# Performance work log

Hardware: AMD Instinct MI355X
Metric: run time of the kernel (lower is better)

Reference implementation:

```python
import jax, jax.numpy as jnp
import numpy as np

EPS = 1e-5
NUM_GROUPS = 32


def group_norm(x, scale, bias):
    # x: [B, C, H, W], 32 groups, normalized over (C/G, H, W)
    B, C, H, W = x.shape
    G = NUM_GROUPS
    xg = x.reshape(B, G, C // G, H, W)
    mean = xg.mean(axis=(2, 3, 4), keepdims=True)
    var = xg.var(axis=(2, 3, 4), keepdims=True)
    xg = (xg - mean) * jax.lax.rsqrt(var + EPS)
    x = xg.reshape(B, C, H, W)
    return x * scale[None, :, None, None] + bias[None, :, None, None]


def setup_inputs() -> dict:
    key = jax.random.key(0)
    ks = jax.random.split(key, 6)
    B, C, H, W = 32, 512, 32, 32
    std = 1.0 / np.sqrt(C)
    return {
        "x": jax.random.normal(ks[0], (B, C, H, W), dtype=jnp.float32),
        "gn_scale": jnp.ones((C,), dtype=jnp.float32),
        "gn_bias": jnp.zeros((C,), dtype=jnp.float32),
        "wq": jax.random.normal(ks[1], (C, C), dtype=jnp.float32) * std,
        "bq": jnp.zeros((C,), dtype=jnp.float32),
        "wk": jax.random.normal(ks[2], (C, C), dtype=jnp.float32) * std,
        "bk": jnp.zeros((C,), dtype=jnp.float32),
        "wv": jax.random.normal(ks[3], (C, C), dtype=jnp.float32) * std,
        "bv": jnp.zeros((C,), dtype=jnp.float32),
        "wo": jax.random.normal(ks[4], (C, C), dtype=jnp.float32) * std,
        "bo": jnp.zeros((C,), dtype=jnp.float32),
    }


def reference(x, gn_scale, gn_bias, wq, bq, wk, bk, wv, bv, wo, bo):
    B, C, H, W = x.shape
    h = group_norm(x, gn_scale, gn_bias)
    # 1x1 convs == per-pixel matmuls; flatten spatial to tokens: [B, HW, C]
    ht = h.reshape(B, C, H * W).transpose(0, 2, 1)
    q = jnp.einsum('bnc,oc->bno', ht, wq) + bq  # [B, HW, C]
    k = jnp.einsum('bnc,oc->bno', ht, wk) + bk
    v = jnp.einsum('bnc,oc->bno', ht, wv) + bv
    scale = 1.0 / jnp.sqrt(jnp.asarray(C, x.dtype))
    w = jnp.einsum('bnc,bmc->bnm', q, k) * scale  # [B, HW, HW]
    w = jax.nn.softmax(w, axis=-1)
    a = jnp.einsum('bnm,bmc->bnc', w, v)  # [B, HW, C]
    out = jnp.einsum('bnc,oc->bno', a, wo) + bo
    out = out.transpose(0, 2, 1).reshape(B, C, H, W)
    return x + out
```

## Files before the change

### kernel.cpp

```cpp
#include <hip/hip_runtime.h>
#include <hip/hip_bf16.h>
#include <stdint.h>

typedef unsigned short u16;
typedef __attribute__((ext_vector_type(8))) short short8;
typedef __attribute__((ext_vector_type(4))) short s16x4;
typedef __attribute__((ext_vector_type(4))) float f32x4;

#define NTOK 1024
#define CDIM 512
#define NG 32

#define GLOAD_LDS16(gptr, lptr)                                                              \
  __builtin_amdgcn_global_load_lds((const __attribute__((address_space(1))) unsigned int*)(gptr), \
                                   (__attribute__((address_space(3))) unsigned int*)(lptr), 16, 0, 0)

__device__ __forceinline__ u16 f2bf(float f) {
  __hip_bfloat16 h = __float2bfloat16(f);
  union { __hip_bfloat16 h; u16 u; } v; v.h = h;
  return v.u;
}

__device__ __forceinline__ float bf2f(u16 b) {
  union { uint32_t u; float f; } v; v.u = ((uint32_t)b) << 16;
  return v.f;
}

__global__ __launch_bounds__(256) void prep_stats(const float* __restrict__ x,
                                                  const float* __restrict__ wq, const float* __restrict__ wk,
                                                  const float* __restrict__ wv, const float* __restrict__ wo,
                                                  const float* __restrict__ bq, const float* __restrict__ bk,
                                                  const float* __restrict__ bv,
                                                  u16* __restrict__ wout, float* __restrict__ bqkv,
                                                  float* __restrict__ rsum,
                                                  float* __restrict__ mean_o, float* __restrict__ rstd_o) {
  int bg = blockIdx.x;
  int i = bg * 256 + threadIdx.x;
  wout[i]          = f2bf(wq[i]);
  wout[262144 + i] = f2bf(wk[i]);
  wout[524288 + i] = f2bf(wv[i]);
  wout[786432 + i] = f2bf(wo[i]);
  if (i < 512) bqkv[i] = bq[i];
  else if (i < 1024) bqkv[i] = bk[i - 512];
  else if (i < 1536) bqkv[i] = bv[i - 1024];
  if (i < 32768) rsum[i] = 0.f;

  const float4* base = (const float4*)(x + (size_t)bg * 16384);
  float s = 0.f, ss = 0.f;
  for (int k = threadIdx.x; k < 4096; k += 256) {
    float4 v = base[k];
    s  += v.x + v.y + v.z + v.w;
    ss += v.x * v.x + v.y * v.y + v.z * v.z + v.w * v.w;
  }
#pragma unroll
  for (int d = 1; d < 64; d <<= 1) { s += __shfl_xor(s, d); ss += __shfl_xor(ss, d); }
  __shared__ float as[4], as2[4];
  int w = threadIdx.x >> 6;
  if ((threadIdx.x & 63) == 0) { as[w] = s; as2[w] = ss; }
  __syncthreads();
  if (threadIdx.x == 0) {
    float S = as[0] + as[1] + as[2] + as[3];
    float SS = as2[0] + as2[1] + as2[2] + as2[3];
    float m = S * (1.f / 16384.f);
    float var = SS * (1.f / 16384.f) - m * m;
    mean_o[bg] = m;
    rstd_o[bg] = rsqrtf(var + 1e-5f);
  }
}

__global__ __launch_bounds__(256) void gn_apply(const float* __restrict__ x,
                                                const float* __restrict__ mean_, const float* __restrict__ rstd_,
                                                const float* __restrict__ gsc, const float* __restrict__ gbi,
                                                u16* __restrict__ h) {
  int n0 = blockIdx.x * 64, c0 = blockIdx.y * 64, b = blockIdx.z;
  __shared__ u16 t[64][65];
  int tid = threadIdx.x;
  int nl4 = (tid & 15) * 4;
  int clb = tid >> 4;
#pragma unroll
  for (int p = 0; p < 4; ++p) {
    int cl = p * 16 + clb;
    int c = c0 + cl;
    int g = c >> 4;
    float m = mean_[b * NG + g], rs = rstd_[b * NG + g];
    float sc = gsc[c] * rs, bi = gbi[c] - m * sc;
    float4 v = *(const float4*)(x + ((size_t)b * CDIM + c) * NTOK + n0 + nl4);
    t[cl][nl4 + 0] = f2bf(v.x * sc + bi);
    t[cl][nl4 + 1] = f2bf(v.y * sc + bi);
    t[cl][nl4 + 2] = f2bf(v.z * sc + bi);
    t[cl][nl4 + 3] = f2bf(v.w * sc + bi);
  }
  __syncthreads();
  int nl = tid >> 3;
  int cc = (tid & 7) * 8;
#pragma unroll
  for (int p = 0; p < 2; ++p) {
    int n = nl + p * 32;
    short8 o;
#pragma unroll
    for (int i = 0; i < 8; ++i) o[i] = (short)t[cc + i][n];
    *(short8*)(h + (size_t)(b * NTOK + n0 + n) * CDIM + c0 + cc) = o;
  }
}

template <int MODE>
__device__ __forceinline__ void gemm_body(const u16* __restrict__ A, const u16* __restrict__ B,
                                          const float* __restrict__ bias, u16* __restrict__ outb,
                                          u16* __restrict__ outb2,
                                          float* __restrict__ outf, const float* __restrict__ resid,
                                          int Ka, int Kb, int nkt,
                                          size_t strideA, size_t strideB, int batch0) {
  int nx = gridDim.x, ny = gridDim.y;
  int nwg = nx * ny * gridDim.z;
  int id = blockIdx.x + nx * (blockIdx.y + ny * blockIdx.z);
  int cpx = nwg >> 3;
  int sw = (id & 7) * cpx + (id >> 3);
  int bx = sw % nx; int t_ = sw / nx;
  int by = t_ % ny; int z = t_ / ny;

  const u16* Amat = A + (size_t)z * strideA;
  const u16* Bmat = B + (size_t)z * strideB;
  int n0 = bx * 256, m0 = by * 256;
  __shared__ __align__(16) u16 SH[65536];
  int tid = threadIdx.x;
  int l = tid & 63, wid = tid >> 6;
  int lr = l & 15, lh = l >> 4;
  int wm = (wid >> 2) * 128;
  int wn = (wid & 3) * 64;

  f32x4 acc[8][4];
#pragma unroll
  for (int i = 0; i < 8; ++i)
#pragma unroll
    for (int j = 0; j < 4; ++j) acc[i][j] = (f32x4){0.f, 0.f, 0.f, 0.f};

  short8 af[4][2];
  short8 bf01[2][2];
  short8 bf23[2][2];

  int sr = tid >> 3, sc = tid & 7;
  int sg = (sc ^ (sr & 7)) << 3;
  const u16* Ag0 = Amat + (size_t)(m0 + sr) * Ka + sg;
  const u16* Ag1 = Ag0 + (size_t)64 * Ka;
  const u16* Bg0 = Bmat + (size_t)(n0 + sr) * Kb + sg;
  const u16* Bg1 = Bg0 + (size_t)64 * Kb;
  size_t hA = (size_t)128 * Ka, hB = (size_t)128 * Kb;
  u16* Al0 = SH + sr * 64 + sc * 8;
  u16* Bl0 = SH + 32768 + sr * 64 + sc * 8;

#define STAGE_A(bufsel, ktv, half)                                        \
  {                                                                       \
    size_t go_ = (size_t)(ktv) * 64 + ((half) ? hA : (size_t)0);          \
    u16* ld_ = Al0 + (bufsel) * 16384 + (half) * 8192;                    \
    GLOAD_LDS16(Ag0 + go_, ld_);                                          \
    GLOAD_LDS16(Ag1 + go_, ld_ + 4096);                                   \
  }
#define STAGE_B(bufsel, ktv, half)                                        \
  {                                                                       \
    size_t go_ = (size_t)(ktv) * 64 + ((half) ? hB : (size_t)0);          \
    u16* ld_ = Bl0 + (bufsel) * 16384 + (half) * 8192;                    \
    GLOAD_LDS16(Bg0 + go_, ld_);                                          \
    GLOAD_LDS16(Bg1 + go_, ld_ + 4096);                                   \
  }

#define READ_AF(ihalf, bufsel)                                                        \
  _Pragma("unroll") for (int i_ = 0; i_ < 4; ++i_) {                                  \
    int row_ = wm + (ihalf) * 64 + i_ * 16 + lr;                                      \
    const u16* p_ = SH + (bufsel) * 16384 + row_ * 64;                                \
    _Pragma("unroll") for (int ks_ = 0; ks_ < 2; ++ks_)                               \
      af[i_][ks_] = *(const short8*)(p_ + (((ks_ * 4 + lh) ^ (row_ & 7)) << 3));      \
  }

#define READ_BF(dst, jbase, bufsel)                                                   \
  _Pragma("unroll") for (int j_ = 0; j_ < 2; ++j_) {                                  \
    int row_ = wn + ((jbase) + j_) * 16 + lr;                                         \
    const u16* p_ = SH + 32768 + (bufsel) * 16384 + row_ * 64;                        \
    _Pragma("unroll") for (int ks_ = 0; ks_ < 2; ++ks_)                               \
      dst[j_][ks_] = *(const short8*)(p_ + (((ks_ * 4 + lh) ^ (row_ & 7)) << 3));     \
  }

#define MFMA_Q(ihalf, jbase, bsrc)                                                    \
  _Pragma("unroll") for (int ks_ = 0; ks_ < 2; ++ks_)                                 \
    _Pragma("unroll") for (int i_ = 0; i_ < 4; ++i_)                                  \
      _Pragma("unroll") for (int j_ = 0; j_ < 2; ++j_)                                \
        acc[(ihalf) * 4 + i_][(jbase) + j_] = __builtin_amdgcn_mfma_f32_16x16x32_bf16( \
            af[i_][ks_], bsrc[j_][ks_], acc[(ihalf) * 4 + i_][(jbase) + j_], 0, 0, 0);

#define PBAR() __builtin_amdgcn_s_barrier()

#define PHASES(BC, BN, GI, DOHI, DOLO)                                    \
  {                                                                       \
    int g1_ = (GI) + 1, g2_ = (GI) + 2;                                   \
                                           \
    READ_AF(0, BC);                                                       \
    READ_BF(bf01, 0, BC);                                                 \
    if (DOHI) { STAGE_A(BN, g1_, 1); }                                    \
    PBAR();                                                               \
    __builtin_amdgcn_s_setprio(1);                                        \
    MFMA_Q(0, 0, bf01);                                                   \
    __builtin_amdgcn_s_setprio(0);                                        \
    PBAR();                                                               \
                                           \
    READ_BF(bf23, 2, BC);                                                 \
    if (DOHI) { STAGE_B(BN, g1_, 1); }                                    \
    PBAR();                                                               \
    __builtin_amdgcn_s_setprio(1);                                        \
    MFMA_Q(0, 2, bf23);                                                   \
    __builtin_amdgcn_s_setprio(0);                                        \
    PBAR();                                                               \
     \
    READ_AF(1, BC);                                                       \
    if (DOLO) { STAGE_B(BC, g2_, 0); }                                    \
    PBAR();                                                               \
    __builtin_amdgcn_s_setprio(1);                                        \
    MFMA_Q(1, 2, bf23);                                                   \
    __builtin_amdgcn_s_setprio(0);                                        \
    PBAR();                                                               \
     \
    if (DOLO) { STAGE_A(BC, g2_, 0); }                                    \
    PBAR();                                                               \
    __builtin_amdgcn_s_setprio(1);                                        \
    MFMA_Q(1, 0, bf01);                                                   \
    __builtin_amdgcn_s_setprio(0);                                        \
    if (DOLO) { asm volatile("s_waitcnt vmcnt(4)"); }                     \
    else      { asm volatile("s_waitcnt vmcnt(0)"); }                     \
    __builtin_amdgcn_sched_barrier(0);                                    \
    PBAR();                                                               \
  }

  int k1 = (1 < nkt) ? 1 : 0;
  STAGE_B(0, 0, 0);
  STAGE_A(0, 0, 0);
  STAGE_A(0, 0, 1);
  STAGE_B(0, 0, 1);
  STAGE_B(1, k1, 0);
  STAGE_A(1, k1, 0);
  asm volatile("s_waitcnt vmcnt(4)");
  __builtin_amdgcn_sched_barrier(0);
  PBAR();

  for (int kt = 0; kt < nkt; kt += 2) {
    int more = (kt + 2 < nkt) ? 1 : 0;
    PHASES(0, 1, kt, 1, more);
    PHASES(1, 0, kt + 1, more, more);
  }

  __syncthreads();
  const int gr0 = m0 + wm, gc0 = n0 + wn;
  u16* eb = SH + wid * 4352;

  if constexpr (MODE == 5) {
    float bj[4];
#pragma unroll
    for (int j = 0; j < 4; ++j) bj[j] = bias[gc0 + j * 16 + lr];
    if (n0 < 1024) {
#pragma unroll
      for (int pass = 0; pass < 2; ++pass) {
#pragma unroll
        for (int i2 = 0; i2 < 4; ++i2)
#pragma unroll
          for (int j = 0; j < 4; ++j)
#pragma unroll
            for (int r = 0; r < 4; ++r)
              eb[(i2 * 16 + lh * 4 + r) * 68 + j * 16 + lr] =
                  f2bf(acc[pass * 4 + i2][j][r] + bj[j]);
        asm volatile("s_waitcnt lgkmcnt(0)");
        __builtin_amdgcn_sched_barrier(0);
#pragma unroll
        for (int t = 0; t < 8; ++t) {
          int row = t * 8 + (l >> 3), c8 = (l & 7) * 8;
          s16x4 lo = *(const s16x4*)(eb + row * 68 + c8);
          s16x4 hi = *(const s16x4*)(eb + row * 68 + c8 + 4);
          short8 o;
          o[0] = lo[0]; o[1] = lo[1]; o[2] = lo[2]; o[3] = lo[3];
          o[4] = hi[0]; o[5] = hi[1]; o[6] = hi[2]; o[7] = hi[3];
          *(short8*)(outb + (size_t)(gr0 + pass * 64 + row) * 1024 + gc0 + c8) = o;
        }
        asm volatile("s_waitcnt lgkmcnt(0)");
        __builtin_amdgcn_sched_barrier(0);
      }
    } else {
      int ch0 = gc0 - 1024;
      int bt = m0 >> 10, tok0 = (m0 & 1023) + wm;
#pragma unroll
      for (int pass = 0; pass < 2; ++pass) {
#pragma unroll
        for (int i2 = 0; i2 < 4; ++i2)
#pragma unroll
          for (int j = 0; j < 4; ++j) {
            s16x4 w;
#pragma unroll
            for (int r = 0; r < 4; ++r)
              w[r] = (short)f2bf(acc[pass * 4 + i2][j][r] + bj[j]);
            *(s16x4*)(eb + (j * 16 + lr) * 68 + i2 * 16 + lh * 4) = w;
          }
        asm volatile("s_waitcnt lgkmcnt(0)");
        __builtin_amdgcn_sched_barrier(0);
#pragma unroll
        for (int t = 0; t < 8; ++t) {
          int row = t * 8 + (l >> 3), c8 = (l & 7) * 8;
          s16x4 lo = *(const s16x4*)(eb + row * 68 + c8);
          s16x4 hi = *(const s16x4*)(eb + row * 68 + c8 + 4);
          short8 o;
          o[0] = lo[0]; o[1] = lo[1]; o[2] = lo[2]; o[3] = lo[3];
          o[4] = hi[0]; o[5] = hi[1]; o[6] = hi[2]; o[7] = hi[3];
          *(short8*)(outb2 + (size_t)(bt * 512 + ch0 + row) * 1024 + tok0 + pass * 64 + c8) = o;
        }
        asm volatile("s_waitcnt lgkmcnt(0)");
        __builtin_amdgcn_sched_barrier(0);
      }
    }
  } else if constexpr (MODE == 3) {
    const float k2 = 0.063758716f;
    u16* obase = outb + (size_t)z * 1048576;
    float* rsb = outf + (size_t)z * 1024;
#pragma unroll
    for (int pass = 0; pass < 2; ++pass) {
#pragma unroll
      for (int i2 = 0; i2 < 4; ++i2)
#pragma unroll
        for (int r = 0; r < 4; ++r) {
          float rp = 0.f;
#pragma unroll
          for (int j = 0; j < 4; ++j) {
            float e = exp2f(acc[pass * 4 + i2][j][r] * k2);
            rp += e;
            eb[(i2 * 16 + lh * 4 + r) * 68 + j * 16 + lr] = f2bf(e);
          }
          rp += __shfl_xor(rp, 1);
          rp += __shfl_xor(rp, 2);
          rp += __shfl_xor(rp, 4);
          rp += __shfl_xor(rp, 8);
          if (lr == 0) atomicAdd(rsb + gr0 + pass * 64 + i2 * 16 + lh * 4 + r, rp);
        }
      asm volatile("s_waitcnt lgkmcnt(0)");
      __builtin_amdgcn_sched_barrier(0);
#pragma unroll
      for (int t = 0; t < 8; ++t) {
        int row = t * 8 + (l >> 3), c8 = (l & 7) * 8;
        s16x4 lo = *(const s16x4*)(eb + row * 68 + c8);
        s16x4 hi = *(const s16x4*)(eb + row * 68 + c8 + 4);
        short8 o;
        o[0] = lo[0]; o[1] = lo[1]; o[2] = lo[2]; o[3] = lo[3];
        o[4] = hi[0]; o[5] = hi[1]; o[6] = hi[2]; o[7] = hi[3];
        *(short8*)(obase + (size_t)(gr0 + pass * 64 + row) * 1024 + gc0 + c8) = o;
      }
      asm volatile("s_waitcnt lgkmcnt(0)");
      __builtin_amdgcn_sched_barrier(0);
    }
  } else if constexpr (MODE == 4) {
    const float* rsg = outf + (size_t)z * 1024;
    u16* obase = outb + (size_t)(batch0 + z) * 524288;
#pragma unroll
    for (int pass = 0; pass < 2; ++pass) {
#pragma unroll
      for (int i2 = 0; i2 < 4; ++i2)
#pragma unroll
        for (int r = 0; r < 4; ++r) {
          float inv_ = 1.f / rsg[gr0 + pass * 64 + i2 * 16 + lh * 4 + r];
#pragma unroll
          for (int j = 0; j < 4; ++j)
            eb[(i2 * 16 + lh * 4 + r) * 68 + j * 16 + lr] =
                f2bf(acc[pass * 4 + i2][j][r] * inv_);
        }
      asm volatile("s_waitcnt lgkmcnt(0)");
      __builtin_amdgcn_sched_barrier(0);
#pragma unroll
      for (int t = 0; t < 8; ++t) {
        int row = t * 8 + (l >> 3), c8 = (l & 7) * 8;
        s16x4 lo = *(const s16x4*)(eb + row * 68 + c8);
        s16x4 hi = *(const s16x4*)(eb + row * 68 + c8 + 4);
        short8 o;
        o[0] = lo[0]; o[1] = lo[1]; o[2] = lo[2]; o[3] = lo[3];
        o[4] = hi[0]; o[5] = hi[1]; o[6] = hi[2]; o[7] = hi[3];
        *(short8*)(obase + (size_t)(gr0 + pass * 64 + row) * 512 + gc0 + c8) = o;
      }
      asm volatile("s_waitcnt lgkmcnt(0)");
      __builtin_amdgcn_sched_barrier(0);
    }
  }
#undef STAGE_A
#undef STAGE_B
#undef READ_AF
#undef READ_BF
#undef MFMA_Q
#undef PBAR
#undef PHASES
}

__device__ __forceinline__ void gemm_body_o(const u16* __restrict__ A, const u16* __restrict__ B,
                                            const float* __restrict__ bias,
                                            float* __restrict__ outf, const float* __restrict__ resid,
                                            int Ka, int Kb, int nkt) {
  int nx = gridDim.x, ny = gridDim.y;
  int nwg = nx * ny;
  int id = blockIdx.x + nx * blockIdx.y;
  int cpx = nwg >> 3;
  int sw = (id & 7) * cpx + (id >> 3);
  int bx = sw % nx; int by = sw / nx;

  int n0 = bx * 128, m0 = by * 256;
  __shared__ __align__(16) u16 SH[36864];
  int tid = threadIdx.x;
  int l = tid & 63, wid = tid >> 6;
  int lr = l & 15, lh = l >> 4;
  int wm = (wid >> 1) * 128;
  int wn = (wid & 1) * 64;

  f32x4 acc[8][4];
#pragma unroll
  for (int i = 0; i < 8; ++i)
#pragma unroll
    for (int j = 0; j < 4; ++j) acc[i][j] = (f32x4){0.f, 0.f, 0.f, 0.f};

  short8 af[8];
  short8 bfr[4];

  int sr = tid >> 2, sc4 = tid & 3;
  int sg = (sc4 ^ ((sr >> 1) & 3)) * 8;
  const u16* Ag0 = A + (size_t)(m0 + sr) * Ka + sg;
  const u16* Bg0 = B + (size_t)(n0 + sr) * Kb + sg;
  u16* Al0 = SH + sr * 32 + sc4 * 8;
  u16* Bl0 = SH + 24576 + sr * 32 + sc4 * 8;

  int rch = (lh ^ ((lr >> 1) & 3)) * 8;

#define STG(bufsel, ktv)                                                          \
  {                                                                               \
    GLOAD_LDS16(Ag0 + (ktv) * 32,                       Al0 + (bufsel) * 8192);   \
    GLOAD_LDS16(Ag0 + (ktv) * 32 + (size_t)64  * Ka,    Al0 + (bufsel) * 8192 + 2048); \
    GLOAD_LDS16(Ag0 + (ktv) * 32 + (size_t)128 * Ka,    Al0 + (bufsel) * 8192 + 4096); \
    GLOAD_LDS16(Ag0 + (ktv) * 32 + (size_t)192 * Ka,    Al0 + (bufsel) * 8192 + 6144); \
    GLOAD_LDS16(Bg0 + (ktv) * 32,                       Bl0 + (bufsel) * 4096);   \
    GLOAD_LDS16(Bg0 + (ktv) * 32 + (size_t)64  * Kb,    Bl0 + (bufsel) * 4096 + 2048); \
  }

#define RDF(bufsel)                                                                   \
  _Pragma("unroll") for (int i_ = 0; i_ < 8; ++i_)                                    \
    af[i_] = *(const short8*)(SH + (bufsel) * 8192 + (wm + i_ * 16 + lr) * 32 + rch); \
  _Pragma("unroll") for (int j_ = 0; j_ < 4; ++j_)                                    \
    bfr[j_] = *(const short8*)(SH + 24576 + (bufsel) * 4096 + (wn + j_ * 16 + lr) * 32 + rch);

#define MFM32()                                                                       \
  _Pragma("unroll") for (int i_ = 0; i_ < 8; ++i_)                                    \
    _Pragma("unroll") for (int j_ = 0; j_ < 4; ++j_)                                  \
      acc[i_][j_] = __builtin_amdgcn_mfma_f32_16x16x32_bf16(af[i_], bfr[j_], acc[i_][j_], 0, 0, 0);

  STG(0, 0);
  STG(1, 1);
  asm volatile("s_waitcnt vmcnt(6)");
  __builtin_amdgcn_sched_barrier(0);
  __builtin_amdgcn_s_barrier();

  int bc = 0, bs = 2;
  for (int t = 0; t < nkt; ++t) {
    const bool more = (t + 2 < nkt);
    if (more) STG(bs, t + 2);
    RDF(bc);
    __builtin_amdgcn_s_setprio(1);
    MFM32();
    __builtin_amdgcn_s_setprio(0);
    if (more) { asm volatile("s_waitcnt vmcnt(6)"); }
    else      { asm volatile("s_waitcnt vmcnt(0)"); }
    __builtin_amdgcn_sched_barrier(0);
    __builtin_amdgcn_s_barrier();
    bc = (bc == 2) ? 0 : bc + 1;
    bs = (bs == 2) ? 0 : bs + 1;
  }

  __syncthreads();
  const int gr0 = m0 + wm, gc0 = n0 + wn;
  float* ebf = (float*)SH + wid * 2176;
  int bt = n0 >> 10, nn0 = (n0 & 1023) + wn;
#pragma unroll
  for (int pass = 0; pass < 4; ++pass) {
#pragma unroll
    for (int i2 = 0; i2 < 2; ++i2)
#pragma unroll
      for (int r = 0; r < 4; ++r) {
        float bv = bias[gr0 + pass * 32 + i2 * 16 + lh * 4 + r];
#pragma unroll
        for (int j = 0; j < 4; ++j)
          ebf[(i2 * 16 + lh * 4 + r) * 68 + j * 16 + lr] = acc[pass * 2 + i2][j][r] + bv;
      }
    asm volatile("s_waitcnt lgkmcnt(0)");
    __builtin_amdgcn_sched_barrier(0);
#pragma unroll
    for (int t = 0; t < 8; ++t) {
      int row = t * 4 + (l >> 4), c4 = (l & 15) * 4;
      float4 vv = *(const float4*)(ebf + row * 68 + c4);
      size_t addr = ((size_t)bt * 512 + gr0 + pass * 32 + row) * 1024 + nn0 + c4;
      const float4 rr = *(const float4*)(resid + addr);
      vv.x += rr.x; vv.y += rr.y; vv.z += rr.z; vv.w += rr.w;
      *(float4*)(outf + addr) = vv;
    }
    asm volatile("s_waitcnt lgkmcnt(0)");
    __builtin_amdgcn_sched_barrier(0);
  }
#undef STG
#undef RDF
#undef MFM32
}

__global__ __launch_bounds__(512, 2) void gemm_qkv(const u16* A, const u16* B, const float* bias,
                                                   u16* outb, u16* outb2, float* outf, const float* resid,
                                                   int Ka, int Kb, int nkt, size_t sA, size_t sB, int b0) {
  gemm_body<5>(A, B, bias, outb, outb2, outf, resid, Ka, Kb, nkt, sA, sB, b0);
}
__global__ __launch_bounds__(256, 2) void gemm_o(const u16* A, const u16* B, const float* bias,
                                                 float* outf, const float* resid,
                                                 int Ka, int Kb, int nkt) {
  gemm_body_o(A, B, bias, outf, resid, Ka, Kb, nkt);
}
__global__ __launch_bounds__(512, 2) void gemm_s(const u16* A, const u16* B, const float* bias,
                                                 u16* outb, u16* outb2, float* outf, const float* resid,
                                                 int Ka, int Kb, int nkt, size_t sA, size_t sB, int b0) {
  gemm_body<3>(A, B, bias, outb, outb2, outf, resid, Ka, Kb, nkt, sA, sB, b0);
}
__global__ __launch_bounds__(512, 2) void gemm_pv(const u16* A, const u16* B, const float* bias,
                                                  u16* outb, u16* outb2, float* outf, const float* resid,
                                                  int Ka, int Kb, int nkt, size_t sA, size_t sB, int b0) {
  gemm_body<4>(A, B, bias, outb, outb2, outf, resid, Ka, Kb, nkt, sA, sB, b0);
}

extern "C" void kernel_launch(void* const* d_in, const int* in_sizes, int n_in,
                              void* d_out, int out_size, void* d_ws, size_t ws_size,
                              hipStream_t stream) {
  const float* x   = (const float*)d_in[0];
  const float* gsc = (const float*)d_in[1];
  const float* gbi = (const float*)d_in[2];
  const float* wq  = (const float*)d_in[3];
  const float* bq  = (const float*)d_in[4];
  const float* wk  = (const float*)d_in[5];
  const float* bk  = (const float*)d_in[6];
  const float* wv  = (const float*)d_in[7];
  const float* bv  = (const float*)d_in[8];
  const float* wo  = (const float*)d_in[9];
  const float* bo  = (const float*)d_in[10];

  char* ws = (char*)d_ws;
  u16* wbf = (u16*)ws;
  float* bqkv = (float*)(ws + (2ull << 20));
  float* mean_ = (float*)(ws + (2ull << 20) + 65536);
  float* rstd_ = mean_ + 1024;
  float* rsum = (float*)(ws + (3ull << 20));
  u16* h   = (u16*)(ws + (4ull << 20));
  u16* qk  = (u16*)(ws + (36ull << 20));
  u16* vm  = (u16*)(ws + (100ull << 20));
  u16* S   = (u16*)(ws + (132ull << 20));
  u16* am  = h;
  float* out = (float*)d_out;

  size_t sbytes = ws_size > (132ull << 20) ? ws_size - (132ull << 20) : 0;
  int CB = 1;
  while (CB < 32 && (size_t)(CB * 2) * (2ull << 20) <= sbytes) CB *= 2;

  prep_stats<<<1024, 256, 0, stream>>>(x, wq, wk, wv, wo, bq, bk, bv, wbf, bqkv, rsum, mean_, rstd_);
  gn_apply<<<dim3(16, 8, 32), 256, 0, stream>>>(x, mean_, rstd_, gsc, gbi, h);
  gemm_qkv<<<dim3(6, 128), 512, 0, stream>>>(h, wbf, bqkv, qk, vm, nullptr, nullptr,
                                             512, 512, 8, 0, 0, 0);
  for (int c0 = 0; c0 < 32; c0 += CB) {
    gemm_s<<<dim3(4, 4, CB), 512, 0, stream>>>(qk + (size_t)c0 * 1048576, qk + 512 + (size_t)c0 * 1048576,
                                               nullptr, S, nullptr, rsum + (size_t)c0 * 1024, nullptr,
                                               1024, 1024, 8, 1048576, 1048576, 0);
    gemm_pv<<<dim3(2, 4, CB), 512, 0, stream>>>(S, vm + (size_t)c0 * 524288,
                                                nullptr, am, nullptr, rsum + (size_t)c0 * 1024, nullptr,
                                                1024, 1024, 16, 1048576, 524288, c0);
  }
  gemm_o<<<dim3(256, 2), 256, 0, stream>>>(wbf + 786432, am, bo, out, x, 512, 512, 16);
}
```

Measured before the change: 225.1 us.

## Fuse QK^T, exp, row-sum and PV into one flash-style attention kernel

Replaces the separate score GEMM (writing bf16 exp scores to a workspace) and PV GEMM with a single fused kernel that keeps 64-query tiles of Q in LDS, streams K and V tiles, computes exp scores and row sums locally, and accumulates P·V in registers. This removes the global round-trip of the 32x1024x1024 score matrix and the per-chunk launch loop. It uses no running max, as before, and the small 16x32 score tiles per wave with many barriers may limit MFMA utilisation.

Measured after the change: 332.8 us. 1.48x slower.

```diff
diff --git a/kernel.cpp b/kernel.cpp
--- a/kernel.cpp
+++ b/kernel.cpp
@@ -32,7 +32,6 @@
                                                   const float* __restrict__ bq, const float* __restrict__ bk,
                                                   const float* __restrict__ bv,
                                                   u16* __restrict__ wout, float* __restrict__ bqkv,
-                                                  float* __restrict__ rsum,
                                                   float* __restrict__ mean_o, float* __restrict__ rstd_o) {
   int bg = blockIdx.x;
   int i = bg * 256 + threadIdx.x;
@@ -43,7 +42,6 @@
   if (i < 512) bqkv[i] = bq[i];
   else if (i < 1024) bqkv[i] = bk[i - 512];
   else if (i < 1536) bqkv[i] = bv[i - 1024];
-  if (i < 32768) rsum[i] = 0.f;
 
   const float4* base = (const float4*)(x + (size_t)bg * 16384);
   float s = 0.f, ss = 0.f;
@@ -107,19 +105,14 @@
 __device__ __forceinline__ void gemm_body(const u16* __restrict__ A, const u16* __restrict__ B,
                                           const float* __restrict__ bias, u16* __restrict__ outb,
                                           u16* __restrict__ outb2,
-                                          float* __restrict__ outf, const float* __restrict__ resid,
-                                          int Ka, int Kb, int nkt,
-                                          size_t strideA, size_t strideB, int batch0) {
+                                          int Ka, int Kb, int nkt) {
   int nx = gridDim.x, ny = gridDim.y;
-  int nwg = nx * ny * gridDim.z;
-  int id = blockIdx.x + nx * (blockIdx.y + ny * blockIdx.z);
+  int nwg = nx * ny;
+  int id = blockIdx.x + nx * blockIdx.y;
   int cpx = nwg >> 3;
   int sw = (id & 7) * cpx + (id >> 3);
-  int bx = sw % nx; int t_ = sw / nx;
-  int by = t_ % ny; int z = t_ / ny;
-
-  const u16* Amat = A + (size_t)z * strideA;
-  const u16* Bmat = B + (size_t)z * strideB;
+  int bx = sw % nx; int by = sw / nx;
+
   int n0 = bx * 256, m0 = by * 256;
   __shared__ __align__(16) u16 SH[65536];
   int tid = threadIdx.x;
@@ -140,9 +133,9 @@
 
   int sr = tid >> 3, sc = tid & 7;
   int sg = (sc ^ (sr & 7)) << 3;
-  const u16* Ag0 = Amat + (size_t)(m0 + sr) * Ka + sg;
+  const u16* Ag0 = A + (size_t)(m0 + sr) * Ka + sg;
   const u16* Ag1 = Ag0 + (size_t)64 * Ka;
-  const u16* Bg0 = Bmat + (size_t)(n0 + sr) * Kb + sg;
+  const u16* Bg0 = B + (size_t)(n0 + sr) * Kb + sg;
   const u16* Bg1 = Bg0 + (size_t)64 * Kb;
   size_t hA = (size_t)128 * Ka, hB = (size_t)128 * Kb;
   u16* Al0 = SH + sr * 64 + sc * 8;
@@ -191,7 +184,6 @@
 #define PHASES(BC, BN, GI, DOHI, DOLO)                                    \
   {                                                                       \
     int g1_ = (GI) + 1, g2_ = (GI) + 2;                                   \
-                                           \
     READ_AF(0, BC);                                                       \
     READ_BF(bf01, 0, BC);                                                 \
     if (DOHI) { STAGE_A(BN, g1_, 1); }                                    \
@@ -200,7 +192,6 @@
     MFMA_Q(0, 0, bf01);                                                   \
     __builtin_amdgcn_s_setprio(0);                                        \
     PBAR();                                                               \
-                                           \
     READ_BF(bf23, 2, BC);                                                 \
     if (DOHI) { STAGE_B(BN, g1_, 1); }                                    \
     PBAR();                                                               \
@@ -208,7 +199,6 @@
     MFMA_Q(0, 2, bf23);                                                   \
     __builtin_amdgcn_s_setprio(0);                                        \
     PBAR();                                                               \
-     \
     READ_AF(1, BC);                                                       \
     if (DOLO) { STAGE_B(BC, g2_, 0); }                                    \
     PBAR();                                                               \
@@ -216,7 +206,6 @@
     MFMA_Q(1, 2, bf23);                                                   \
     __builtin_amdgcn_s_setprio(0);                                        \
     PBAR();                                                               \
-     \
     if (DOLO) { STAGE_A(BC, g2_, 0); }                                    \
     PBAR();                                                               \
     __builtin_amdgcn_s_setprio(1);                                        \
@@ -249,90 +238,20 @@
   const int gr0 = m0 + wm, gc0 = n0 + wn;
   u16* eb = SH + wid * 4352;
 
-  if constexpr (MODE == 5) {
-    float bj[4];
-#pragma unroll
-    for (int j = 0; j < 4; ++j) bj[j] = bias[gc0 + j * 16 + lr];
-    if (n0 < 1024) {
-#pragma unroll
-      for (int pass = 0; pass < 2; ++pass) {
-#pragma unroll
-        for (int i2 = 0; i2 < 4; ++i2)
-#pragma unroll
-          for (int j = 0; j < 4; ++j)
-#pragma unroll
-            for (int r = 0; r < 4; ++r)
-              eb[(i2 * 16 + lh * 4 + r) * 68 + j * 16 + lr] =
-                  f2bf(acc[pass * 4 + i2][j][r] + bj[j]);
-        asm volatile("s_waitcnt lgkmcnt(0)");
-        __builtin_amdgcn_sched_barrier(0);
-#pragma unroll
-        for (int t = 0; t < 8; ++t) {
-          int row = t * 8 + (l >> 3), c8 = (l & 7) * 8;
-          s16x4 lo = *(const s16x4*)(eb + row * 68 + c8);
-          s16x4 hi = *(const s16x4*)(eb + row * 68 + c8 + 4);
-          short8 o;
-          o[0] = lo[0]; o[1] = lo[1]; o[2] = lo[2]; o[3] = lo[3];
-          o[4] = hi[0]; o[5] = hi[1]; o[6] = hi[2]; o[7] = hi[3];
-          *(short8*)(outb + (size_t)(gr0 + pass * 64 + row) * 1024 + gc0 + c8) = o;
-        }
-        asm volatile("s_waitcnt lgkmcnt(0)");
-        __builtin_amdgcn_sched_barrier(0);
-      }
-    } else {
-      int ch0 = gc0 - 1024;
-      int bt = m0 >> 10, tok0 = (m0 & 1023) + wm;
-#pragma unroll
-      for (int pass = 0; pass < 2; ++pass) {
-#pragma unroll
-        for (int i2 = 0; i2 < 4; ++i2)
-#pragma unroll
-          for (int j = 0; j < 4; ++j) {
-            s16x4 w;
-#pragma unroll
-            for (int r = 0; r < 4; ++r)
-              w[r] = (short)f2bf(acc[pass * 4 + i2][j][r] + bj[j]);
-            *(s16x4*)(eb + (j * 16 + lr) * 68 + i2 * 16 + lh * 4) = w;
-          }
-        asm volatile("s_waitcnt lgkmcnt(0)");
-        __builtin_amdgcn_sched_barrier(0);
-#pragma unroll
-        for (int t = 0; t < 8; ++t) {
-          int row = t * 8 + (l >> 3), c8 = (l & 7) * 8;
-          s16x4 lo = *(const s16x4*)(eb + row * 68 + c8);
-          s16x4 hi = *(const s16x4*)(eb + row * 68 + c8 + 4);
-          short8 o;
-          o[0] = lo[0]; o[1] = lo[1]; o[2] = lo[2]; o[3] = lo[3];
-          o[4] = hi[0]; o[5] = hi[1]; o[6] = hi[2]; o[7] = hi[3];
-          *(short8*)(outb2 + (size_t)(bt * 512 + ch0 + row) * 1024 + tok0 + pass * 64 + c8) = o;
-        }
-        asm volatile("s_waitcnt lgkmcnt(0)");
-        __builtin_amdgcn_sched_barrier(0);
-      }
-    }
-  } else if constexpr (MODE == 3) {
-    const float k2 = 0.063758716f;
-    u16* obase = outb + (size_t)z * 1048576;
-    float* rsb = outf + (size_t)z * 1024;
+  float bj[4];
+#pragma unroll
+  for (int j = 0; j < 4; ++j) bj[j] = bias[gc0 + j * 16 + lr];
+  if (n0 < 1024) {
 #pragma unroll
     for (int pass = 0; pass < 2; ++pass) {
 #pragma unroll
       for (int i2 = 0; i2 < 4; ++i2)
 #pragma unroll
-        for (int r = 0; r < 4; ++r) {
-          float rp = 0.f;
-#pragma unroll
-          for (int j = 0; j < 4; ++j) {
-            float e = exp2f(acc[pass * 4 + i2][j][r] * k2);
-            rp += e;
-            eb[(i2 * 16 + lh * 4 + r) * 68 + j * 16 + lr] = f2bf(e);
-          }
-          rp += __shfl_xor(rp, 1);
-          rp += __shfl_xor(rp, 2);
-          rp += __shfl_xor(rp, 4);
-          rp += __shfl_xor(rp, 8);
-          if (lr == 0) atomicAdd(rsb + gr0 + pass * 64 + i2 * 16 + lh * 4 + r, rp);
-        }
+        for (int j = 0; j < 4; ++j)
+#pragma unroll
+          for (int r = 0; r < 4; ++r)
+            eb[(i2 * 16 + lh * 4 + r) * 68 + j * 16 + lr] =
+                f2bf(acc[pass * 4 + i2][j][r] + bj[j]);
       asm volatile("s_waitcnt lgkmcnt(0)");
       __builtin_amdgcn_sched_barrier(0);
 #pragma unroll
@@ -343,25 +262,25 @@
         short8 o;
         o[0] = lo[0]; o[1] = lo[1]; o[2] = lo[2]; o[3] = lo[3];
         o[4] = hi[0]; o[5] = hi[1]; o[6] = hi[2]; o[7] = hi[3];
-        *(short8*)(obase + (size_t)(gr0 + pass * 64 + row) * 1024 + gc0 + c8) = o;
+        *(short8*)(outb + (size_t)(gr0 + pass * 64 + row) * 1024 + gc0 + c8) = o;
       }
       asm volatile("s_waitcnt lgkmcnt(0)");
       __builtin_amdgcn_sched_barrier(0);
     }
-  } else if constexpr (MODE == 4) {
-    const float* rsg = outf + (size_t)z * 1024;
-    u16* obase = outb + (size_t)(batch0 + z) * 524288;
+  } else {
+    int ch0 = gc0 - 1024;
+    int bt = m0 >> 10, tok0 = (m0 & 1023) + wm;
 #pragma unroll
     for (int pass = 0; pass < 2; ++pass) {
 #pragma unroll
       for (int i2 = 0; i2 < 4; ++i2)
 #pragma unroll
-        for (int r = 0; r < 4; ++r) {
-          float inv_ = 1.f / rsg[gr0 + pass * 64 + i2 * 16 + lh * 4 + r];
-#pragma unroll
-          for (int j = 0; j < 4; ++j)
-            eb[(i2 * 16 + lh * 4 + r) * 68 + j * 16 + lr] =
-                f2bf(acc[pass * 4 + i2][j][r] * inv_);
+        for (int j = 0; j < 4; ++j) {
+          s16x4 w;
+#pragma unroll
+          for (int r = 0; r < 4; ++r)
+            w[r] = (short)f2bf(acc[pass * 4 + i2][j][r] + bj[j]);
+          *(s16x4*)(eb + (j * 16 + lr) * 68 + i2 * 16 + lh * 4) = w;
         }
       asm volatile("s_waitcnt lgkmcnt(0)");
       __builtin_amdgcn_sched_barrier(0);
@@ -373,7 +292,7 @@
         short8 o;
         o[0] = lo[0]; o[1] = lo[1]; o[2] = lo[2]; o[3] = lo[3];
         o[4] = hi[0]; o[5] = hi[1]; o[6] = hi[2]; o[7] = hi[3];
-        *(short8*)(obase + (size_t)(gr0 + pass * 64 + row) * 512 + gc0 + c8) = o;
+        *(short8*)(outb2 + (size_t)(bt * 512 + ch0 + row) * 1024 + tok0 + pass * 64 + c8) = o;
       }
       asm volatile("s_waitcnt lgkmcnt(0)");
       __builtin_amdgcn_sched_barrier(0);
@@ -502,25 +421,174 @@
 #undef MFM32
 }
 
+__global__ __launch_bounds__(512, 2) void attn_fused(const u16* __restrict__ qk,
+                                                     const u16* __restrict__ vm,
+                                                     u16* __restrict__ am) {
+  int id = blockIdx.x + 32 * blockIdx.y;
+  int sw = (id & 7) * 64 + (id >> 3);
+  int b = sw & 31; int qt = sw >> 5;
+
+  __shared__ __align__(16) u16 SH[67712];
+  float* rsum_l = (float*)(SH + 67584);
+
+  int tid = threadIdx.x;
+  int l = tid & 63, wid = tid >> 6;
+  int lr = l & 15, lh = l >> 4;
+
+  const u16* qbase = qk + (size_t)(b * 1024 + qt * 64) * 1024;
+  const u16* kbase = qk + (size_t)(b * 1024) * 1024 + 512;
+  const u16* vbase = vm + (size_t)b * 524288;
+
+#define STAGE_KT(ktv)                                                              \
+  {                                                                                \
+    int r_ = tid >> 6, c_ = tid & 63;                                              \
+    _Pragma("unroll") for (int L = 0; L < 4; ++L) {                                \
+      int row_ = L * 8 + r_;                                                       \
+      int gch_ = (c_ & 56) | ((c_ ^ row_) & 7);                                    \
+      GLOAD_LDS16(kbase + (size_t)((ktv) * 32 + row_) * 1024 + gch_ * 8,           \
+                  SH + 32768 + row_ * 512 + c_ * 8);                               \
+    }                                                                              \
+  }
+#define STAGE_VT(ktv)                                                              \
+  {                                                                                \
+    _Pragma("unroll") for (int L = 0; L < 4; ++L) {                                \
+      int row_ = L * 128 + (tid >> 2);                                             \
+      int c_ = tid & 3;                                                            \
+      int gch_ = (c_ ^ row_) & 3;                                                  \
+      GLOAD_LDS16(vbase + (size_t)row_ * 1024 + (ktv) * 32 + gch_ * 8,             \
+                  SH + 51200 + L * 4096 + tid * 8);                                \
+    }                                                                              \
+  }
+
+  STAGE_KT(0);
+  STAGE_VT(0);
+  if (tid < 64) rsum_l[tid] = 0.f;
+#pragma unroll
+  for (int p = 0; p < 8; ++p) {
+    int idx = p * 512 + tid;
+    int row = idx >> 6, ch = idx & 63;
+    short8 v = *(const short8*)(qbase + (size_t)row * 1024 + ch * 8);
+    int sch = (ch & 56) | ((ch ^ row) & 7);
+    *(short8*)(SH + row * 512 + sch * 8) = v;
+  }
+  asm volatile("s_waitcnt lgkmcnt(0)");
+  __builtin_amdgcn_sched_barrier(0);
+
+  f32x4 acco[4][4];
+#pragma unroll
+  for (int i = 0; i < 4; ++i)
+#pragma unroll
+    for (int j = 0; j < 4; ++j) acco[i][j] = (f32x4){0.f, 0.f, 0.f, 0.f};
+
+  int wq = wid >> 1, wk = wid & 1;
+  const u16* qrow = SH + (wq * 16 + lr) * 512;
+  const u16* krow = SH + 32768 + (wk * 16 + lr) * 512;
+  const float k2 = 0.063758716f;
+
+  for (int kt = 0; kt < 32; ++kt) {
+    asm volatile("s_waitcnt vmcnt(4)");
+    __builtin_amdgcn_sched_barrier(0);
+    __builtin_amdgcn_s_barrier();
+    f32x4 accs = (f32x4){0.f, 0.f, 0.f, 0.f};
+#pragma unroll
+    for (int ks = 0; ks < 16; ++ks) {
+      int ch = ks * 4 + lh;
+      int cq = (ch & 56) | ((ch ^ lr) & 7);
+      short8 aq = *(const short8*)(qrow + (cq << 3));
+      short8 bk = *(const short8*)(krow + (cq << 3));
+      accs = __builtin_amdgcn_mfma_f32_16x16x32_bf16(aq, bk, accs, 0, 0, 0);
+    }
+    __builtin_amdgcn_s_barrier();
+    if (kt < 31) STAGE_KT(kt + 1);
+    {
+      int pcol = wk * 16 + lr;
+#pragma unroll
+      for (int r = 0; r < 4; ++r) {
+        float e = exp2f(accs[r] * k2);
+        int prow = wq * 16 + lh * 4 + r;
+        SH[49152 + prow * 32 + (((pcol >> 3) ^ (prow & 3)) << 3) + (pcol & 7)] = f2bf(e);
+        float s = e;
+        s += __shfl_xor(s, 1); s += __shfl_xor(s, 2);
+        s += __shfl_xor(s, 4); s += __shfl_xor(s, 8);
+        if (lr == 0) atomicAdd(rsum_l + prow, s);
+      }
+    }
+    asm volatile("s_waitcnt lgkmcnt(0)");
+    __builtin_amdgcn_sched_barrier(0);
+    __builtin_amdgcn_s_barrier();
+    if (kt < 31) { asm volatile("s_waitcnt vmcnt(4)"); }
+    else         { asm volatile("s_waitcnt vmcnt(0)"); }
+    __builtin_amdgcn_sched_barrier(0);
+    short8 ap[4], bv[4];
+#pragma unroll
+    for (int i = 0; i < 4; ++i) {
+      int prow = i * 16 + lr;
+      ap[i] = *(const short8*)(SH + 49152 + prow * 32 + ((lh ^ (prow & 3)) << 3));
+    }
+#pragma unroll
+    for (int j = 0; j < 4; ++j) {
+      int vrow = wid * 64 + j * 16 + lr;
+      bv[j] = *(const short8*)(SH + 51200 + vrow * 32 + ((lh ^ (vrow & 3)) << 3));
+    }
+    asm volatile("s_waitcnt lgkmcnt(0)");
+    __builtin_amdgcn_sched_barrier(0);
+    __builtin_amdgcn_s_barrier();
+    if (kt < 31) STAGE_VT(kt + 1);
+    __builtin_amdgcn_s_setprio(1);
+#pragma unroll
+    for (int i = 0; i < 4; ++i)
+#pragma unroll
+      for (int j = 0; j < 4; ++j)
+        acco[i][j] = __builtin_amdgcn_mfma_f32_16x16x32_bf16(ap[i], bv[j], acco[i][j], 0, 0, 0);
+    __builtin_amdgcn_s_setprio(0);
+  }
+
+  __builtin_amdgcn_s_barrier();
+  float inv[4][4];
+#pragma unroll
+  for (int i = 0; i < 4; ++i)
+#pragma unroll
+    for (int r = 0; r < 4; ++r)
+      inv[i][r] = 1.f / rsum_l[i * 16 + lh * 4 + r];
+  u16* ob = SH + 51200;
+#pragma unroll
+  for (int p = 0; p < 2; ++p) {
+#pragma unroll
+    for (int i2 = 0; i2 < 2; ++i2) {
+      int i = p * 2 + i2;
+#pragma unroll
+      for (int j = 0; j < 4; ++j)
+#pragma unroll
+        for (int r = 0; r < 4; ++r)
+          ob[(i2 * 16 + lh * 4 + r) * 512 + wid * 64 + j * 16 + lr] =
+              f2bf(acco[i][j][r] * inv[i][r]);
+    }
+    asm volatile("s_waitcnt lgkmcnt(0)");
+    __builtin_amdgcn_sched_barrier(0);
+    __builtin_amdgcn_s_barrier();
+    {
+      int row = tid >> 4, cb = (tid & 15) * 32;
+      u16* gdst = am + (size_t)(b * 1024 + qt * 64 + p * 32 + row) * 512 + cb;
+#pragma unroll
+      for (int s = 0; s < 4; ++s)
+        *(short8*)(gdst + s * 8) = *(const short8*)(ob + row * 512 + cb + s * 8);
+    }
+    asm volatile("s_waitcnt lgkmcnt(0)");
+    __builtin_amdgcn_sched_barrier(0);
+    __builtin_amdgcn_s_barrier();
+  }
+#undef STAGE_KT
+#undef STAGE_VT
+}
+
 __global__ __launch_bounds__(512, 2) void gemm_qkv(const u16* A, const u16* B, const float* bias,
-                                                   u16* outb, u16* outb2, float* outf, const float* resid,
-                                                   int Ka, int Kb, int nkt, size_t sA, size_t sB, int b0) {
-  gemm_body<5>(A, B, bias, outb, outb2, outf, resid, Ka, Kb, nkt, sA, sB, b0);
+                                                   u16* outb, u16* outb2, int Ka, int Kb, int nkt) {
+  gemm_body<5>(A, B, bias, outb, outb2, Ka, Kb, nkt);
 }
 __global__ __launch_bounds__(256, 2) void gemm_o(const u16* A, const u16* B, const float* bias,
                                                  float* outf, const float* resid,
                                                  int Ka, int Kb, int nkt) {
   gemm_body_o(A, B, bias, outf, resid, Ka, Kb, nkt);
-}
-__global__ __launch_bounds__(512, 2) void gemm_s(const u16* A, const u16* B, const float* bias,
-                                                 u16* outb, u16* outb2, float* outf, const float* resid,
-                                                 int Ka, int Kb, int nkt, size_t sA, size_t sB, int b0) {
-  gemm_body<3>(A, B, bias, outb, outb2, outf, resid, Ka, Kb, nkt, sA, sB, b0);
-}
-__global__ __launch_bounds__(512, 2) void gemm_pv(const u16* A, const u16* B, const float* bias,
-                                                  u16* outb, u16* outb2, float* outf, const float* resid,
-                                                  int Ka, int Kb, int nkt, size_t sA, size_t sB, int b0) {
-  gemm_body<4>(A, B, bias, outb, outb2, outf, resid, Ka, Kb, nkt, sA, sB, b0);
 }
 
 extern "C" void kernel_launch(void* const* d_in, const int* in_sizes, int n_in,
@@ -543,29 +611,15 @@
   float* bqkv = (float*)(ws + (2ull << 20));
   float* mean_ = (float*)(ws + (2ull << 20) + 65536);
   float* rstd_ = mean_ + 1024;
-  float* rsum = (float*)(ws + (3ull << 20));
   u16* h   = (u16*)(ws + (4ull << 20));
   u16* qk  = (u16*)(ws + (36ull << 20));
   u16* vm  = (u16*)(ws + (100ull << 20));
-  u16* S   = (u16*)(ws + (132ull << 20));
   u16* am  = h;
   float* out = (float*)d_out;
 
-  size_t sbytes = ws_size > (132ull << 20) ? ws_size - (132ull << 20) : 0;
-  int CB = 1;
-  while (CB < 32 && (size_t)(CB * 2) * (2ull << 20) <= sbytes) CB *= 2;
-
-  prep_stats<<<1024, 256, 0, stream>>>(x, wq, wk, wv, wo, bq, bk, bv, wbf, bqkv, rsum, mean_, rstd_);
+  prep_stats<<<1024, 256, 0, stream>>>(x, wq, wk, wv, wo, bq, bk, bv, wbf, bqkv, mean_, rstd_);
   gn_apply<<<dim3(16, 8, 32), 256, 0, stream>>>(x, mean_, rstd_, gsc, gbi, h);
-  gemm_qkv<<<dim3(6, 128), 512, 0, stream>>>(h, wbf, bqkv, qk, vm, nullptr, nullptr,
-                                             512, 512, 8, 0, 0, 0);
-  for (int c0 = 0; c0 < 32; c0 += CB) {
-    gemm_s<<<dim3(4, 4, CB), 512, 0, stream>>>(qk + (size_t)c0 * 1048576, qk + 512 + (size_t)c0 * 1048576,
-                                               nullptr, S, nullptr, rsum + (size_t)c0 * 1024, nullptr,
-                                               1024, 1024, 8, 1048576, 1048576, 0);
-    gemm_pv<<<dim3(2, 4, CB), 512, 0, stream>>>(S, vm + (size_t)c0 * 524288,
-                                                nullptr, am, nullptr, rsum + (size_t)c0 * 1024, nullptr,
-                                                1024, 1024, 16, 1048576, 524288, c0);
-  }
+  gemm_qkv<<<dim3(6, 128), 512, 0, stream>>>(h, wbf, bqkv, qk, vm, 512, 512, 8);
+  attn_fused<<<dim3(32, 16), 512, 0, stream>>>(qk, vm, am);
   gemm_o<<<dim3(256, 2), 256, 0, stream>>>(wbf + 786432, am, bo, out, x, 512, 512, 16);
 }
```
